# Optimization experiments

Hardware: AMD Instinct MI355X
Metric: run time of the kernel (lower is better)

## Reference

```python
import jax, jax.numpy as jnp
import numpy as np

NODE_CARDS = [119, 5, 12, 12, 10, 6, 6, 2, 2]
EDGE_CARDS = [5, 6, 2]
HIDDEN = 256
LAYERS = 5
N = 60000
E = 180000
G = 2048  # num graphs (fixed num_segments)
BN_EPS = 1e-5

_NODE_OFFS = np.concatenate([[0], np.cumsum(NODE_CARDS[:-1])]).astype(np.int32)
_EDGE_OFFS = np.concatenate([[0], np.cumsum(EDGE_CARDS[:-1])]).astype(np.int32)
_NODE_MAX = np.asarray(NODE_CARDS, np.int32) - 1
_EDGE_MAX = np.asarray(EDGE_CARDS, np.int32) - 1


def _cat_sum(x, table, maxs, offs):
    # x: [N, F] int; table: [sum(cards), H] -> [N, H]
    idx = jnp.clip(x, 0, maxs[None, :]) + offs[None, :]
    return table[idx].sum(axis=1)


def setup_inputs() -> dict:
    key = jax.random.key(0)
    ks = jax.random.split(key, 32)
    w = 0.0625  # ~ xavier for 256

    def nrm(k, shape, s=w):
        return jax.random.normal(k, shape, dtype=jnp.float32) * s

    inp = {
        'x': jax.random.randint(ks[0], (N, len(NODE_CARDS)), 0, 119, dtype=jnp.int32),
        'edge_index': jax.random.randint(ks[1], (2, E), 0, N, dtype=jnp.int32),
        'edge_attr': jax.random.randint(ks[2], (E, len(EDGE_CARDS)), 0, 6, dtype=jnp.int32),
        'batch': jnp.sort(jax.random.randint(ks[3], (N,), 0, G, dtype=jnp.int32)),
        # embeddings
        'node_emb': nrm(ks[4], (int(sum(NODE_CARDS)), HIDDEN), 0.1),
        'edge_emb': nrm(ks[5], (int(sum(EDGE_CARDS)), HIDDEN), 0.1),
        'vn_emb': nrm(ks[6], (1, HIDDEN), 0.1),
        # GINE conv: eps + 2-layer MLP per layer (stacked)
        'eps': jnp.zeros((LAYERS,), jnp.float32),
        'W1': nrm(ks[7], (LAYERS, HIDDEN, HIDDEN)),
        'b1': jnp.zeros((LAYERS, HIDDEN), jnp.float32),
        'W2': nrm(ks[8], (LAYERS, HIDDEN, HIDDEN)),
        'b2': jnp.zeros((LAYERS, HIDDEN), jnp.float32),
        # BatchNorm (eval mode: running stats)
        'bn_gamma': jnp.ones((LAYERS, HIDDEN), jnp.float32),
        'bn_beta': jnp.zeros((LAYERS, HIDDEN), jnp.float32),
        'bn_mean': nrm(ks[9], (LAYERS, HIDDEN), 0.02),
        'bn_var': jnp.ones((LAYERS, HIDDEN), jnp.float32),
        # virtual-node MLP per layer
        'vW1': nrm(ks[10], (LAYERS, HIDDEN, HIDDEN)),
        'vb1': jnp.zeros((LAYERS, HIDDEN), jnp.float32),
        'vW2': nrm(ks[11], (LAYERS, HIDDEN, HIDDEN)),
        'vb2': jnp.zeros((LAYERS, HIDDEN), jnp.float32),
        # head MLP (2 layers: hidden->hidden->1)
        'hW1': nrm(ks[12], (HIDDEN, HIDDEN)),
        'hb1': jnp.zeros((HIDDEN,), jnp.float32),
        'hW2': nrm(ks[13], (HIDDEN, 1)),
        'hb2': jnp.zeros((1,), jnp.float32),
    }
    return inp


def reference(x, edge_index, edge_attr, batch,
              node_emb, edge_emb, vn_emb, eps,
              W1, b1, W2, b2,
              bn_gamma, bn_beta, bn_mean, bn_var,
              vW1, vb1, vW2, vb2,
              hW1, hb1, hW2, hb2):
    node_maxs = jnp.asarray(_NODE_MAX)
    node_offs = jnp.asarray(_NODE_OFFS)
    edge_maxs = jnp.asarray(_EDGE_MAX)
    edge_offs = jnp.asarray(_EDGE_OFFS)

    h = _cat_sum(x, node_emb, node_maxs, node_offs)          # [N, H]
    ea = _cat_sum(edge_attr, edge_emb, edge_maxs, edge_offs)  # [E, H]
    src, dst = edge_index[0], edge_index[1]

    vn = jnp.broadcast_to(vn_emb[0], (G, HIDDEN))  # [G, H]

    def mean_pool(h_):
        s = jax.ops.segment_sum(h_, batch, num_segments=G)
        cnt = jax.ops.segment_sum(jnp.ones((h_.shape[0], 1), h_.dtype), batch, num_segments=G)
        return s / jnp.maximum(cnt, 1.0)

    for l in range(LAYERS):
        h = h + vn[batch]
        # GINEConv: msg = relu(x_src + edge_attr); agg scatter-add onto dst
        msg = jax.nn.relu(h[src] + ea)                        # [E, H]
        agg = jax.ops.segment_sum(msg, dst, num_segments=N)   # [N, H]
        z = (1.0 + eps[l]) * h + agg
        z = jax.nn.relu(z @ W1[l] + b1[l]) @ W2[l] + b2[l]
        # BatchNorm1d (eval, running stats)
        z = (z - bn_mean[l]) * (bn_gamma[l] / jnp.sqrt(bn_var[l] + BN_EPS)) + bn_beta[l]
        h = jax.nn.relu(z)
        # virtual-node update
        g = mean_pool(h)
        vn = vn + (jax.nn.relu(g @ vW1[l] + vb1[l]) @ vW2[l] + vb2[l])

    g = mean_pool(h)                                          # [G, H]
    logits = (jax.nn.relu(g @ hW1 + hb1) @ hW2 + hb2).reshape(-1)  # [G]
    return logits
```

## Files before the change

### kernel.cpp

```cpp
#include <hip/hip_runtime.h>

#define NN 60000
#define NE 180000
#define NG 2048
#define NL 5
#define CAP 32

typedef unsigned short u16;
typedef unsigned int u32;
typedef __bf16 bf16x8 __attribute__((ext_vector_type(8)));
typedef float f32x4 __attribute__((ext_vector_type(4)));

__device__ __forceinline__ u16 f2bf(float f) {
    u32 u = __builtin_bit_cast(u32, f);
    u += 0x7FFFu + ((u >> 16) & 1u);
    return (u16)(u >> 16);
}
__device__ __forceinline__ float bf2f(u16 s) {
    return __builtin_bit_cast(float, (u32)s << 16);
}
__device__ __forceinline__ void gload_lds16(const void* g, void* l) {
    __builtin_amdgcn_global_load_lds(
        (const __attribute__((address_space(1))) unsigned int*)g,
        (__attribute__((address_space(3))) unsigned int*)l, 16, 0, 0);
}

__constant__ int NODE_OFF[9]  = {0, 119, 124, 136, 148, 158, 164, 170, 172};
__constant__ int NODE_MAXC[9] = {118, 4, 11, 11, 9, 5, 5, 1, 1};

__global__ __launch_bounds__(256) void k_prep_weights(
    const float* __restrict__ W1, const float* __restrict__ W2,
    const float* __restrict__ vW1, const float* __restrict__ vW2,
    const float* __restrict__ hW1, u16* __restrict__ Wt)
{
    int mat = blockIdx.x >> 8;
    int n = blockIdx.x & 255;
    int k = threadIdx.x;
    const float* src;
    if (mat < 5)       src = W1 + (size_t)mat * 65536;
    else if (mat < 10) src = W2 + (size_t)(mat - 5) * 65536;
    else if (mat < 15) src = vW1 + (size_t)(mat - 10) * 65536;
    else if (mat < 20) src = vW2 + (size_t)(mat - 15) * 65536;
    else               src = hW1;
    Wt[(size_t)mat * 65536 + n * 256 + k] = f2bf(src[k * 256 + n]);
}

__global__ __launch_bounds__(256) void k_misc(
    const float* __restrict__ eemb, const int* __restrict__ batch,
    const float* __restrict__ vn_emb,
    u16* __restrict__ comb, int* __restrict__ starts,
    float* __restrict__ vn, u16* __restrict__ vnbf, float* __restrict__ gsum)
{
    int b = blockIdx.x;
    if (b < 2048) {
        int i = b * 256 + threadIdx.x;
        float v = vn_emb[i & 255];
        vn[i] = v;
        vnbf[i] = f2bf(v);
        gsum[i] = 0.f;
    } else if (b < 2108) {
        int r = b - 2048, c = threadIdx.x;
        int a0 = r / 12, a1 = (r % 12) / 2, a2 = r & 1;
        comb[r * 256 + c] = f2bf(eemb[a0 * 256 + c] + eemb[(5 + a1) * 256 + c] +
                                 eemb[(11 + a2) * 256 + c]);
    } else {
        int g = (b - 2108) * 256 + threadIdx.x;
        if (g > NG) return;
        int lo = 0, hi = NN;
        while (lo < hi) {
            int mid = (lo + hi) >> 1;
            if (batch[mid] < g) lo = mid + 1; else hi = mid;
        }
        starts[g] = lo;
    }
}

__global__ __launch_bounds__(256) void k_embed(const int* __restrict__ x,
                                               const float* __restrict__ node_emb,
                                               u16* __restrict__ hbf,
                                               int* __restrict__ deg)
{
    int i = blockIdx.x * 4 + (threadIdx.x >> 6);
    if (i >= NN) return;
    if ((threadIdx.x & 63) == 0) deg[i] = 0;
    int c = (threadIdx.x & 63) * 4;
    float4 s = make_float4(0.f, 0.f, 0.f, 0.f);
#pragma unroll
    for (int f = 0; f < 9; ++f) {
        int xv = x[i * 9 + f];
        xv = xv < 0 ? 0 : (xv > NODE_MAXC[f] ? NODE_MAXC[f] : xv);
        const float4 t = *(const float4*)&node_emb[(size_t)(NODE_OFF[f] + xv) * 256 + c];
        s.x += t.x; s.y += t.y; s.z += t.z; s.w += t.w;
    }
    ushort4 o;
    o.x = f2bf(s.x); o.y = f2bf(s.y); o.z = f2bf(s.z); o.w = f2bf(s.w);
    *(ushort4*)&hbf[(size_t)i * 256 + c] = o;
}

__global__ __launch_bounds__(256) void k_bucket(
    const int* __restrict__ src, const int* __restrict__ dst,
    const int* __restrict__ eattr, int* __restrict__ deg, u32* __restrict__ slots)
{
    int e = blockIdx.x * 256 + threadIdx.x;
    if (e >= NE) return;
    int a0 = eattr[e * 3 + 0]; a0 = a0 < 0 ? 0 : (a0 > 4 ? 4 : a0);
    int a1 = eattr[e * 3 + 1]; a1 = a1 < 0 ? 0 : (a1 > 5 ? 5 : a1);
    int a2 = eattr[e * 3 + 2]; a2 = a2 < 0 ? 0 : (a2 > 1 ? 1 : a2);
    u32 code = (u32)(a0 * 12 + a1 * 2 + a2);
    int d = dst[e];
    int p = atomicAdd(&deg[d], 1);
    if (p < CAP) slots[(size_t)d * CAP + p] = (u32)src[e] | (code << 17);
}

__device__ __forceinline__ void stageW(const u16* __restrict__ W, u16* Bl,
                                       int k0, int tid, int wid)
{
#pragma unroll
    for (int i = 0; i < 4; ++i) {
        int slot = i * 512 + tid;
        int row = slot >> 3, cch = slot & 7;
        int g = cch ^ (row & 7);
        gload_lds16((const char*)W + (size_t)row * 512 + (size_t)k0 * 2 + (g << 4),
                    (char*)Bl + ((i * 512 + wid * 64) << 4));
    }
}

__device__ __forceinline__ void gemm64(const u16* Tl, u16* Bl, const u16* __restrict__ W,
                                       f32x4 (&acc)[2][4], int wm, int wn,
                                       int lane, int tid, int wid)
{
    const int cl = lane & 15;
    for (int k0 = 0; k0 < 256; k0 += 64) {
        __syncthreads();
        stageW(W, Bl, k0, tid, wid);
        __syncthreads();
#pragma unroll
        for (int kw = 0; kw < 2; ++kw) {
            int q = kw * 4 + (lane >> 4);
            int qt = (k0 >> 3) + q;
            bf16x8 af[2], bfr[4];
#pragma unroll
            for (int t = 0; t < 2; ++t) {
                int ar = wm + t * 16 + cl;
                af[t] = __builtin_bit_cast(bf16x8,
                    *(const uint4*)((const char*)Tl + (ar << 9) + ((qt ^ (ar & 7)) << 4)));
            }
#pragma unroll
            for (int t = 0; t < 4; ++t) {
                int br = wn + t * 16 + cl;
                bfr[t] = __builtin_bit_cast(bf16x8,
                    *(const uint4*)((const char*)Bl + (br << 7) + ((q ^ (br & 7)) << 4)));
            }
#pragma unroll
            for (int i = 0; i < 2; ++i)
#pragma unroll
                for (int j = 0; j < 4; ++j)
                    acc[i][j] = __builtin_amdgcn_mfma_f32_16x16x32_bf16(af[i], bfr[j], acc[i][j], 0, 0, 0);
        }
    }
}

__device__ __forceinline__ void writeT(u16* Tl, const f32x4 (&acc)[2][4],
                                       const float* __restrict__ b1,
                                       int wm, int wn, int lane)
{
    const int cl = lane & 15, rg = lane >> 4;
#pragma unroll
    for (int j = 0; j < 4; ++j) {
        int col = wn + j * 16 + cl;
        float bv = b1[col];
#pragma unroll
        for (int i = 0; i < 2; ++i)
#pragma unroll
            for (int r = 0; r < 4; ++r) {
                int row = wm + i * 16 + rg * 4 + r;
                float v = fmaxf(acc[i][j][r] + bv, 0.f);
                *(u16*)((char*)Tl + (row << 9) + ((((col >> 3) ^ (row & 7))) << 4) +
                        ((col & 7) << 1)) = f2bf(v);
            }
    }
}

__global__ __launch_bounds__(512) void k_mlpA(
    const u16* __restrict__ hcur, u16* __restrict__ hnxt,
    const u16* __restrict__ vnbf, const int* __restrict__ batch,
    const u32* __restrict__ slots, const int* __restrict__ deg,
    const u16* __restrict__ comb, const float* __restrict__ epsp,
    const u16* __restrict__ W1t, const u16* __restrict__ W2t,
    const float* __restrict__ b1, const float* __restrict__ b2,
    const float* __restrict__ bng, const float* __restrict__ bnb,
    const float* __restrict__ bnm, const float* __restrict__ bnv,
    float* __restrict__ gsum)
{
    __shared__ __align__(16) u16 Bl[256 * 64];
    __shared__ __align__(16) u16 Tl[64 * 256];
    __shared__ int batchLds[64];
    const int m0 = blockIdx.x * 64;
    const int tid = threadIdx.x, lane = tid & 63, wid = tid >> 6;
    const int wm = (wid >> 2) * 32, wn = (wid & 3) * 64;
    const int cl = lane & 15, rg = lane >> 4;

    if (tid < 64) batchLds[tid] = (m0 + tid < NN) ? batch[m0 + tid] : -1;

    {
        const float ep = 1.0f + *epsp;
        const int c = lane * 4;
#pragma unroll
        for (int n = 0; n < 8; ++n) {
            int d = m0 + wid * 8 + n;
            ushort4 o = make_ushort4(0, 0, 0, 0);
            if (d < NN) {
                int nd = deg[d]; nd = nd > CAP ? CAP : nd;
                const u32* sl = slots + (size_t)d * CAP;
                u32 sv_l = (lane < nd) ? sl[lane] : 0u;
                int b_l = (lane < nd) ? batch[sv_l & 0x1FFFFu] : 0;
                float4 acc = make_float4(0.f, 0.f, 0.f, 0.f);
                for (int p = 0; p < nd; ++p) {
                    u32 sv = (u32)__shfl((int)sv_l, p);
                    int b  = __shfl(b_l, p);
                    int s  = (int)(sv & 0x1FFFFu);
                    int code = (int)(sv >> 17);
                    const ushort4 hv = *(const ushort4*)&hcur[(size_t)s * 256 + c];
                    const ushort4 vv = *(const ushort4*)&vnbf[(size_t)b * 256 + c];
                    const ushort4 tv = *(const ushort4*)&comb[(size_t)code * 256 + c];
                    acc.x += fmaxf(bf2f(hv.x) + bf2f(vv.x) + bf2f(tv.x), 0.f);
                    acc.y += fmaxf(bf2f(hv.y) + bf2f(vv.y) + bf2f(tv.y), 0.f);
                    acc.z += fmaxf(bf2f(hv.z) + bf2f(vv.z) + bf2f(tv.z), 0.f);
                    acc.w += fmaxf(bf2f(hv.w) + bf2f(vv.w) + bf2f(tv.w), 0.f);
                }
                int bd = batch[d];
                const ushort4 hd = *(const ushort4*)&hcur[(size_t)d * 256 + c];
                const ushort4 vd = *(const ushort4*)&vnbf[(size_t)bd * 256 + c];
                o.x = f2bf((bf2f(hd.x) + bf2f(vd.x)) * ep + acc.x);
                o.y = f2bf((bf2f(hd.y) + bf2f(vd.y)) * ep + acc.y);
                o.z = f2bf((bf2f(hd.z) + bf2f(vd.z)) * ep + acc.z);
                o.w = f2bf((bf2f(hd.w) + bf2f(vd.w)) * ep + acc.w);
            }
            int row = wid * 8 + n;
            *(ushort4*)((char*)Tl + (row << 9) + ((((c >> 3) ^ (row & 7))) << 4) +
                        ((c & 7) << 1)) = o;
        }
    }
    __syncthreads();

    f32x4 acc1[2][4] = {};
    gemm64(Tl, Bl, W1t, acc1, wm, wn, lane, tid, wid);
    __syncthreads();
    writeT(Tl, acc1, b1, wm, wn, lane);

    f32x4 acc2[2][4] = {};
    gemm64(Tl, Bl, W2t, acc2, wm, wn, lane, tid, wid);
    __syncthreads();

#pragma unroll
    for (int j = 0; j < 4; ++j) {
        int gn = wn + j * 16 + cl;
        float bv = b2[gn];
        float sc = bng[gn] * rsqrtf(bnv[gn] + 1e-5f);
        float sh = bnb[gn] - bnm[gn] * sc;
#pragma unroll
        for (int i = 0; i < 2; ++i) {
#pragma unroll
            for (int r = 0; r < 4; ++r) {
                int lr = wm + i * 16 + rg * 4 + r;
                int gm = m0 + lr;
                if (gm >= NN) continue;
                float v = acc2[i][j][r] + bv;
                u16 hb = f2bf(fmaxf(v * sc + sh, 0.f));
                hnxt[(size_t)gm * 256 + gn] = hb;
                Tl[lr * 256 + gn] = hb;
            }
        }
    }
    __syncthreads();

    {
        int col = tid & 255, half = tid >> 8;
        float s = 0.f;
        int gcur = -1;
        int r0 = half * 32;
        for (int r = r0; r < r0 + 32; ++r) {
            int g = batchLds[r];
            if (g < 0) break;
            if (g != gcur) {
                if (gcur >= 0) atomicAdd(&gsum[(size_t)gcur * 256 + col], s);
                gcur = g; s = 0.f;
            }
            s += bf2f(Tl[r * 256 + col]);
        }
        if (gcur >= 0) atomicAdd(&gsum[(size_t)gcur * 256 + col], s);
    }
}

__global__ __launch_bounds__(512) void k_vnmlp(
    float* __restrict__ gsum, const int* __restrict__ starts,
    const u16* __restrict__ W1t, const u16* __restrict__ W2t,
    const float* __restrict__ b1, const float* __restrict__ b2,
    float* __restrict__ vn, u16* __restrict__ vnbf)
{
    __shared__ __align__(16) u16 Bl[256 * 64];
    __shared__ __align__(16) u16 Tl[64 * 256];
    const int m0 = blockIdx.x * 64;
    const int tid = threadIdx.x, lane = tid & 63, wid = tid >> 6;
    const int wm = (wid >> 2) * 32, wn = (wid & 3) * 64;
    const int cl = lane & 15, rg = lane >> 4;

    {
        const int c = lane * 4;
#pragma unroll
        for (int n = 0; n < 8; ++n) {
            int row = wid * 8 + n;
            int g = m0 + row;
            float4 sv = *(const float4*)&gsum[(size_t)g * 256 + c];
            *(float4*)&gsum[(size_t)g * 256 + c] = make_float4(0.f, 0.f, 0.f, 0.f);
            float cnt = (float)(starts[g + 1] - starts[g]);
            float inv = 1.0f / fmaxf(cnt, 1.0f);
            ushort4 o;
            o.x = f2bf(sv.x * inv); o.y = f2bf(sv.y * inv);
            o.z = f2bf(sv.z * inv); o.w = f2bf(sv.w * inv);
            *(ushort4*)((char*)Tl + (row << 9) + ((((c >> 3) ^ (row & 7))) << 4) +
                        ((c & 7) << 1)) = o;
        }
    }
    __syncthreads();

    f32x4 acc1[2][4] = {};
    gemm64(Tl, Bl, W1t, acc1, wm, wn, lane, tid, wid);
    __syncthreads();
    writeT(Tl, acc1, b1, wm, wn, lane);

    f32x4 acc2[2][4] = {};
    gemm64(Tl, Bl, W2t, acc2, wm, wn, lane, tid, wid);

#pragma unroll
    for (int j = 0; j < 4; ++j) {
        int gn = wn + j * 16 + cl;
        float bv = b2[gn];
#pragma unroll
        for (int i = 0; i < 2; ++i) {
#pragma unroll
            for (int r = 0; r < 4; ++r) {
                int gm = m0 + wm + i * 16 + rg * 4 + r;
                size_t idx = (size_t)gm * 256 + gn;
                float nv = vn[idx] + acc2[i][j][r] + bv;
                vn[idx] = nv;
                vnbf[idx] = f2bf(nv);
            }
        }
    }
}

__global__ __launch_bounds__(512) void k_headf(
    const float* __restrict__ gsum, const int* __restrict__ starts,
    const u16* __restrict__ W1t, const float* __restrict__ b1,
    const float* __restrict__ hW2, const float* __restrict__ hb2,
    float* __restrict__ out)
{
    __shared__ __align__(16) u16 Bl[256 * 64];
    __shared__ __align__(16) u16 Tl[64 * 256];
    const int m0 = blockIdx.x * 64;
    const int tid = threadIdx.x, lane = tid & 63, wid = tid >> 6;
    const int wm = (wid >> 2) * 32, wn = (wid & 3) * 64;

    {
        const int c = lane * 4;
#pragma unroll
        for (int n = 0; n < 8; ++n) {
            int row = wid * 8 + n;
            int g = m0 + row;
            float4 sv = *(const float4*)&gsum[(size_t)g * 256 + c];
            float cnt = (float)(starts[g + 1] - starts[g]);
            float inv = 1.0f / fmaxf(cnt, 1.0f);
            ushort4 o;
            o.x = f2bf(sv.x * inv); o.y = f2bf(sv.y * inv);
            o.z = f2bf(sv.z * inv); o.w = f2bf(sv.w * inv);
            *(ushort4*)((char*)Tl + (row << 9) + ((((c >> 3) ^ (row & 7))) << 4) +
                        ((c & 7) << 1)) = o;
        }
    }
    __syncthreads();

    f32x4 acc1[2][4] = {};
    gemm64(Tl, Bl, W1t, acc1, wm, wn, lane, tid, wid);
    __syncthreads();
    writeT(Tl, acc1, b1, wm, wn, lane);
    __syncthreads();

    int row = tid >> 3, oct = tid & 7;
    float s = 0.f;
#pragma unroll
    for (int c = 0; c < 32; ++c) {
        int col = oct * 32 + c;
        int byte = (row << 9) + ((((col >> 3) ^ (row & 7))) << 4) + ((col & 7) << 1);
        s += bf2f(*(const u16*)((const char*)Tl + byte)) * hW2[col];
    }
    s += __shfl_down(s, 4);
    s += __shfl_down(s, 2);
    s += __shfl_down(s, 1);
    if (oct == 0) out[m0 + row] = s + hb2[0];
}

extern "C" void kernel_launch(void* const* d_in, const int* in_sizes, int n_in,
                              void* d_out, int out_size, void* d_ws, size_t ws_size,
                              hipStream_t stream)
{
    const int*   x        = (const int*)d_in[0];
    const int*   ei       = (const int*)d_in[1];
    const int*   eattr    = (const int*)d_in[2];
    const int*   batch    = (const int*)d_in[3];
    const float* node_emb = (const float*)d_in[4];
    const float* edge_emb = (const float*)d_in[5];
    const float* vn_emb   = (const float*)d_in[6];
    const float* eps      = (const float*)d_in[7];
    const float* W1       = (const float*)d_in[8];
    const float* b1       = (const float*)d_in[9];
    const float* W2       = (const float*)d_in[10];
    const float* b2       = (const float*)d_in[11];
    const float* bng      = (const float*)d_in[12];
    const float* bnb      = (const float*)d_in[13];
    const float* bnm      = (const float*)d_in[14];
    const float* bnv      = (const float*)d_in[15];
    const float* vW1      = (const float*)d_in[16];
    const float* vb1      = (const float*)d_in[17];
    const float* vW2      = (const float*)d_in[18];
    const float* vb2      = (const float*)d_in[19];
    const float* hW1      = (const float*)d_in[20];
    const float* hb1      = (const float*)d_in[21];
    const float* hW2      = (const float*)d_in[22];
    const float* hb2      = (const float*)d_in[23];
    float* out = (float*)d_out;

    char* ws = (char*)d_ws;
    size_t off = 0;
    auto alloc = [&](size_t b) {
        char* p = ws + off;
        off = (off + b + 255) & ~(size_t)255;
        return p;
    };
    u16*   hbf0 = (u16*)alloc((size_t)NN * 256 * 2);
    u16*   hbf1 = (u16*)alloc((size_t)NN * 256 * 2);
    float* vn   = (float*)alloc((size_t)NG * 256 * 4);
    u16*   vnbf = (u16*)alloc((size_t)NG * 256 * 2);
    float* gsum = (float*)alloc((size_t)NG * 256 * 4);
    u16*   Wt   = (u16*)alloc((size_t)21 * 65536 * 2);
    int*   starts = (int*)alloc((size_t)(NG + 1) * 4);
    u16*   comb = (u16*)alloc((size_t)60 * 256 * 2);
    int*   deg  = (int*)alloc((size_t)NN * 4);
    u32*   slots = (u32*)alloc((size_t)NN * CAP * 4);

    const int* srcI = ei;
    const int* dstI = ei + NE;

    k_prep_weights<<<21 * 256, 256, 0, stream>>>(W1, W2, vW1, vW2, hW1, Wt);
    k_misc<<<2117, 256, 0, stream>>>(edge_emb, batch, vn_emb, comb, starts, vn, vnbf, gsum);
    k_embed<<<NN / 4, 256, 0, stream>>>(x, node_emb, hbf0, deg);
    k_bucket<<<(NE + 255) / 256, 256, 0, stream>>>(srcI, dstI, eattr, deg, slots);

    const int GBIG = (NN + 63) / 64;
    const int GSM  = NG / 64;

    u16* hcur = hbf0;
    u16* hnxt = hbf1;
    for (int l = 0; l < NL; ++l) {
        k_mlpA<<<GBIG, 512, 0, stream>>>(hcur, hnxt, vnbf, batch, slots, deg, comb,
                                         eps + l,
                                         Wt + (size_t)(0 + l) * 65536,
                                         Wt + (size_t)(5 + l) * 65536,
                                         b1 + l * 256, b2 + l * 256,
                                         bng + l * 256, bnb + l * 256,
                                         bnm + l * 256, bnv + l * 256,
                                         gsum);
        if (l < NL - 1) {
            k_vnmlp<<<GSM, 512, 0, stream>>>(gsum, starts,
                                             Wt + (size_t)(10 + l) * 65536,
                                             Wt + (size_t)(15 + l) * 65536,
                                             vb1 + l * 256, vb2 + l * 256,
                                             vn, vnbf);
        }
        u16* t = hcur; hcur = hnxt; hnxt = t;
    }
    k_headf<<<GSM, 512, 0, stream>>>(gsum, starts, Wt + (size_t)20 * 65536,
                                     hb1, hW2, hb2, out);
}
```

Before: 601.8 us.

## Split edge aggregation out of fused MLP kernel into standalone gather kernel

Result: faster. 549.2 us (-8.7%).

```diff
diff --git a/kernel.cpp b/kernel.cpp
--- a/kernel.cpp
+++ b/kernel.cpp
@@ -23,6 +23,9 @@
     __builtin_amdgcn_global_load_lds(
         (const __attribute__((address_space(1))) unsigned int*)g,
         (__attribute__((address_space(3))) unsigned int*)l, 16, 0, 0);
+}
+__device__ __forceinline__ int swz(int row, int col) {
+    return (row << 9) + ((((col >> 3) ^ (row & 7))) << 4) + ((col & 7) << 1);
 }
 
 __constant__ int NODE_OFF[9]  = {0, 119, 124, 136, 148, 158, 164, 170, 172};
@@ -112,6 +115,49 @@
     if (p < CAP) slots[(size_t)d * CAP + p] = (u32)src[e] | (code << 17);
 }
 
+__global__ __launch_bounds__(256) void k_agg(
+    const u16* __restrict__ hbf, const u16* __restrict__ vnbf,
+    const int* __restrict__ batch, const u32* __restrict__ slots,
+    const int* __restrict__ deg, const u16* __restrict__ comb,
+    u16* __restrict__ Abf, const float* __restrict__ epsp)
+{
+    int d = blockIdx.x * 4 + (threadIdx.x >> 6);
+    int lane = threadIdx.x & 63;
+    int c = lane * 4;
+    int nd = deg[d];
+    nd = nd > CAP ? CAP : nd;
+
+    const u32* sl = slots + (size_t)d * CAP;
+    u32 sv_l = (lane < nd) ? sl[lane] : 0u;
+    int b_l = (lane < nd) ? batch[sv_l & 0x1FFFFu] : 0;
+
+    float4 acc = make_float4(0.f, 0.f, 0.f, 0.f);
+    for (int p = 0; p < nd; ++p) {
+        u32 sv = (u32)__shfl((int)sv_l, p);
+        int b  = __shfl(b_l, p);
+        int s  = (int)(sv & 0x1FFFFu);
+        int code = (int)(sv >> 17);
+        const ushort4 hv = *(const ushort4*)&hbf[(size_t)s * 256 + c];
+        const ushort4 vv = *(const ushort4*)&vnbf[(size_t)b * 256 + c];
+        const ushort4 tv = *(const ushort4*)&comb[(size_t)code * 256 + c];
+        acc.x += fmaxf(bf2f(hv.x) + bf2f(vv.x) + bf2f(tv.x), 0.f);
+        acc.y += fmaxf(bf2f(hv.y) + bf2f(vv.y) + bf2f(tv.y), 0.f);
+        acc.z += fmaxf(bf2f(hv.z) + bf2f(vv.z) + bf2f(tv.z), 0.f);
+        acc.w += fmaxf(bf2f(hv.w) + bf2f(vv.w) + bf2f(tv.w), 0.f);
+    }
+
+    int bd = batch[d];
+    float ep = 1.0f + *epsp;
+    const ushort4 hd = *(const ushort4*)&hbf[(size_t)d * 256 + c];
+    const ushort4 vd = *(const ushort4*)&vnbf[(size_t)bd * 256 + c];
+    ushort4 o;
+    o.x = f2bf((bf2f(hd.x) + bf2f(vd.x)) * ep + acc.x);
+    o.y = f2bf((bf2f(hd.y) + bf2f(vd.y)) * ep + acc.y);
+    o.z = f2bf((bf2f(hd.z) + bf2f(vd.z)) * ep + acc.z);
+    o.w = f2bf((bf2f(hd.w) + bf2f(vd.w)) * ep + acc.w);
+    *(ushort4*)&Abf[(size_t)d * 256 + c] = o;
+}
+
 __device__ __forceinline__ void stageW(const u16* __restrict__ W, u16* Bl,
                                        int k0, int tid, int wid)
 {
@@ -175,17 +221,14 @@
             for (int r = 0; r < 4; ++r) {
                 int row = wm + i * 16 + rg * 4 + r;
                 float v = fmaxf(acc[i][j][r] + bv, 0.f);
-                *(u16*)((char*)Tl + (row << 9) + ((((col >> 3) ^ (row & 7))) << 4) +
-                        ((col & 7) << 1)) = f2bf(v);
-            }
-    }
-}
-
-__global__ __launch_bounds__(512) void k_mlpA(
-    const u16* __restrict__ hcur, u16* __restrict__ hnxt,
-    const u16* __restrict__ vnbf, const int* __restrict__ batch,
-    const u32* __restrict__ slots, const int* __restrict__ deg,
-    const u16* __restrict__ comb, const float* __restrict__ epsp,
+                *(u16*)((char*)Tl + swz(row, col)) = f2bf(v);
+            }
+    }
+}
+
+__global__ __launch_bounds__(512) void k_mlpP(
+    const u16* __restrict__ Abf, u16* __restrict__ hnxt,
+    const int* __restrict__ batch,
     const u16* __restrict__ W1t, const u16* __restrict__ W2t,
     const float* __restrict__ b1, const float* __restrict__ b2,
     const float* __restrict__ bng, const float* __restrict__ bnb,
@@ -202,46 +245,14 @@
 
     if (tid < 64) batchLds[tid] = (m0 + tid < NN) ? batch[m0 + tid] : -1;
 
-    {
-        const float ep = 1.0f + *epsp;
-        const int c = lane * 4;
-#pragma unroll
-        for (int n = 0; n < 8; ++n) {
-            int d = m0 + wid * 8 + n;
-            ushort4 o = make_ushort4(0, 0, 0, 0);
-            if (d < NN) {
-                int nd = deg[d]; nd = nd > CAP ? CAP : nd;
-                const u32* sl = slots + (size_t)d * CAP;
-                u32 sv_l = (lane < nd) ? sl[lane] : 0u;
-                int b_l = (lane < nd) ? batch[sv_l & 0x1FFFFu] : 0;
-                float4 acc = make_float4(0.f, 0.f, 0.f, 0.f);
-                for (int p = 0; p < nd; ++p) {
-                    u32 sv = (u32)__shfl((int)sv_l, p);
-                    int b  = __shfl(b_l, p);
-                    int s  = (int)(sv & 0x1FFFFu);
-                    int code = (int)(sv >> 17);
-                    const ushort4 hv = *(const ushort4*)&hcur[(size_t)s * 256 + c];
-                    const ushort4 vv = *(const ushort4*)&vnbf[(size_t)b * 256 + c];
-                    const ushort4 tv = *(const ushort4*)&comb[(size_t)code * 256 + c];
-                    acc.x += fmaxf(bf2f(hv.x) + bf2f(vv.x) + bf2f(tv.x), 0.f);
-                    acc.y += fmaxf(bf2f(hv.y) + bf2f(vv.y) + bf2f(tv.y), 0.f);
-                    acc.z += fmaxf(bf2f(hv.z) + bf2f(vv.z) + bf2f(tv.z), 0.f);
-                    acc.w += fmaxf(bf2f(hv.w) + bf2f(vv.w) + bf2f(tv.w), 0.f);
-                }
-                int bd = batch[d];
-                const ushort4 hd = *(const ushort4*)&hcur[(size_t)d * 256 + c];
-                const ushort4 vd = *(const ushort4*)&vnbf[(size_t)bd * 256 + c];
-                o.x = f2bf((bf2f(hd.x) + bf2f(vd.x)) * ep + acc.x);
-                o.y = f2bf((bf2f(hd.y) + bf2f(vd.y)) * ep + acc.y);
-                o.z = f2bf((bf2f(hd.z) + bf2f(vd.z)) * ep + acc.z);
-                o.w = f2bf((bf2f(hd.w) + bf2f(vd.w)) * ep + acc.w);
-            }
-            int row = wid * 8 + n;
-            *(ushort4*)((char*)Tl + (row << 9) + ((((c >> 3) ^ (row & 7))) << 4) +
-                        ((c & 7) << 1)) = o;
-        }
-    }
-    __syncthreads();
+#pragma unroll
+    for (int i = 0; i < 4; ++i) {
+        int slot = i * 512 + tid;
+        int row = slot >> 5, cch = slot & 31;
+        int g = cch ^ (row & 7);
+        gload_lds16((const char*)Abf + (size_t)(m0 + row) * 512 + (g << 4),
+                    (char*)Tl + ((i * 512 + wid * 64) << 4));
+    }
 
     f32x4 acc1[2][4] = {};
     gemm64(Tl, Bl, W1t, acc1, wm, wn, lane, tid, wid);
@@ -268,7 +279,7 @@
                 float v = acc2[i][j][r] + bv;
                 u16 hb = f2bf(fmaxf(v * sc + sh, 0.f));
                 hnxt[(size_t)gm * 256 + gn] = hb;
-                Tl[lr * 256 + gn] = hb;
+                *(u16*)((char*)Tl + swz(lr, gn)) = hb;
             }
         }
     }
@@ -286,7 +297,7 @@
                 if (gcur >= 0) atomicAdd(&gsum[(size_t)gcur * 256 + col], s);
                 gcur = g; s = 0.f;
             }
-            s += bf2f(Tl[r * 256 + col]);
+            s += bf2f(*(const u16*)((const char*)Tl + swz(r, col)));
         }
         if (gcur >= 0) atomicAdd(&gsum[(size_t)gcur * 256 + col], s);
     }
@@ -318,8 +329,7 @@
             ushort4 o;
             o.x = f2bf(sv.x * inv); o.y = f2bf(sv.y * inv);
             o.z = f2bf(sv.z * inv); o.w = f2bf(sv.w * inv);
-            *(ushort4*)((char*)Tl + (row << 9) + ((((c >> 3) ^ (row & 7))) << 4) +
-                        ((c & 7) << 1)) = o;
+            *(ushort4*)((char*)Tl + swz(row, c)) = o;
         }
     }
     __syncthreads();
@@ -374,8 +384,7 @@
             ushort4 o;
             o.x = f2bf(sv.x * inv); o.y = f2bf(sv.y * inv);
             o.z = f2bf(sv.z * inv); o.w = f2bf(sv.w * inv);
-            *(ushort4*)((char*)Tl + (row << 9) + ((((c >> 3) ^ (row & 7))) << 4) +
-                        ((c & 7) << 1)) = o;
+            *(ushort4*)((char*)Tl + swz(row, c)) = o;
         }
     }
     __syncthreads();
@@ -391,8 +400,7 @@
 #pragma unroll
     for (int c = 0; c < 32; ++c) {
         int col = oct * 32 + c;
-        int byte = (row << 9) + ((((col >> 3) ^ (row & 7))) << 4) + ((col & 7) << 1);
-        s += bf2f(*(const u16*)((const char*)Tl + byte)) * hW2[col];
+        s += bf2f(*(const u16*)((const char*)Tl + swz(row, col))) * hW2[col];
     }
     s += __shfl_down(s, 4);
     s += __shfl_down(s, 2);
@@ -439,6 +447,7 @@
     };
     u16*   hbf0 = (u16*)alloc((size_t)NN * 256 * 2);
     u16*   hbf1 = (u16*)alloc((size_t)NN * 256 * 2);
+    u16*   Abf  = (u16*)alloc((size_t)NN * 256 * 2);
     float* vn   = (float*)alloc((size_t)NG * 256 * 4);
     u16*   vnbf = (u16*)alloc((size_t)NG * 256 * 2);
     float* gsum = (float*)alloc((size_t)NG * 256 * 4);
@@ -462,8 +471,8 @@
     u16* hcur = hbf0;
     u16* hnxt = hbf1;
     for (int l = 0; l < NL; ++l) {
-        k_mlpA<<<GBIG, 512, 0, stream>>>(hcur, hnxt, vnbf, batch, slots, deg, comb,
-                                         eps + l,
+        k_agg<<<NN / 4, 256, 0, stream>>>(hcur, vnbf, batch, slots, deg, comb, Abf, eps + l);
+        k_mlpP<<<GBIG, 512, 0, stream>>>(Abf, hnxt, batch,
                                          Wt + (size_t)(0 + l) * 65536,
                                          Wt + (size_t)(5 + l) * 65536,
                                          b1 + l * 256, b2 + l * 256,
```
